# Kernel tuning notes

Hardware: AMD Instinct MI355X
Metric: run time of the kernel (lower is better)

The kernel has to match this reference:

```python
import jax, jax.numpy as jnp
import numpy as np
import itertools
from jax import lax

KERNEL_SIZE = 3
ITERATION = 12
PAD = KERNEL_SIZE // 2
# offsets in the exact order torch code generates them: product([0,1,-1], repeat=2)
OFFSETS = list(itertools.product([*range(KERNEL_SIZE // 2 + 1), *range(-(KERNEL_SIZE // 2), 0)], repeat=2))


def setup_inputs() -> dict:
    key = jax.random.key(0)
    k1, k2, k3, k4 = jax.random.split(key, 4)
    B, C, H, W = 4, 32, 480, 640
    kernel_x = jax.random.normal(k1, (B, C, H, W), jnp.float32)
    x = jax.random.normal(k2, (B, 1, H, W), jnp.float32)
    W_aff = jax.random.normal(k3, (KERNEL_SIZE ** 2 - 1, C, 3, 3), jnp.float32) * 0.05
    b_aff = jax.random.normal(k4, (KERNEL_SIZE ** 2 - 1,), jnp.float32) * 0.05
    return {"kernel_x": kernel_x, "x": x, "W_aff": W_aff, "b_aff": b_aff}


def _gen_kernel(aff):
    # aff: [B, k^2-1, H, W] -> normalized affinity kernel [B, k^2, H, W]
    abs_sum = jnp.sum(jnp.abs(aff), axis=1, keepdims=True)
    a = aff / abs_sum
    s = jnp.sum(a, axis=1, keepdims=True)
    return jnp.concatenate([1.0 - s, a], axis=1)


def _im2col(x):
    # x: [B, 1, H, W] -> shifted copies [B, k^2, H, W] with zero padding,
    # out[:, k, p] = x[:, 0, p - offset_k]
    B, _, H, W = x.shape
    xp = jnp.pad(x[:, 0], ((0, 0), (PAD, PAD), (PAD, PAD)))
    cols = [xp[:, PAD - oi:PAD - oi + H, PAD - oj:PAD - oj + W] for (oi, oj) in OFFSETS]
    return jnp.stack(cols, axis=1)


def reference(kernel_x, x, W_aff, b_aff):
    # affinity_net: 3x3 conv, 32 -> 8 channels, SAME padding
    aff = lax.conv_general_dilated(
        kernel_x, W_aff, window_strides=(1, 1), padding="SAME",
        dimension_numbers=("NCHW", "OIHW", "NCHW"),
    ) + b_aff[None, :, None, None]
    kernel = _gen_kernel(aff)  # [B, 9, H, W]
    for _ in range(ITERATION):
        x = jnp.sum(_im2col(x) * kernel, axis=1, keepdims=True)
    return x
```

## Files before the change

kernel.cpp:

```cpp
#include <hip/hip_runtime.h>
#include <hip/hip_fp16.h>

#define BB 4
#define CC 32
#define HH 480
#define WW 640
#define HWv (HH*WW)

union H8 { __half h[8]; float4 f4; };
union H4 { short4 s; __half h[4]; };

__global__ __launch_bounds__(128) void conv_gen(const float* __restrict__ kx,
                                                const float* __restrict__ Wf,
                                                const float* __restrict__ bf,
                                                __half* __restrict__ K)
{
    int tid = blockIdx.x * 128 + threadIdx.x;
    const int XT = WW / 8;
    int x8 = tid % XT;
    int t2 = tid / XT;
    int y  = t2 % HH;
    int b  = t2 / HH;
    if (b >= BB) return;
    int x0 = x8 * 8;

    float acc[8][8];
#pragma unroll
    for (int o = 0; o < 8; ++o) {
        float bv = bf[o];
#pragma unroll
        for (int p = 0; p < 8; ++p) acc[o][p] = bv;
    }

    const float* kxb = kx + (size_t)b * CC * HWv + (size_t)y * WW + x0;
    const bool xm = (x0 > 0);
    const bool xp = (x0 + 8 < WW);

    for (int c = 0; c < CC; ++c) {
        const float* pl = kxb + (size_t)c * HWv;
#pragma unroll
        for (int r = 0; r < 3; ++r) {
            const int dy = r - 1;
            const bool rowok = (y + dy >= 0) && (y + dy < HH);
            const float* rp = pl + dy * WW;
            float row[10];
            if (rowok) {
                float4 v0 = *reinterpret_cast<const float4*>(rp);
                float4 v1 = *reinterpret_cast<const float4*>(rp + 4);
                row[0] = xm ? rp[-1] : 0.f;
                row[1] = v0.x; row[2] = v0.y; row[3] = v0.z; row[4] = v0.w;
                row[5] = v1.x; row[6] = v1.y; row[7] = v1.z; row[8] = v1.w;
                row[9] = xp ? rp[8] : 0.f;
            } else {
#pragma unroll
                for (int q = 0; q < 10; ++q) row[q] = 0.f;
            }
#pragma unroll
            for (int o = 0; o < 8; ++o) {
#pragma unroll
                for (int t = 0; t < 3; ++t) {
                    float wv = Wf[((o * CC + c) * 3 + r) * 3 + t];
#pragma unroll
                    for (int p = 0; p < 8; ++p) acc[o][p] += wv * row[p + t];
                }
            }
        }
    }

    float k0[8];
#pragma unroll
    for (int p = 0; p < 8; ++p) {
        float asum = 0.f;
#pragma unroll
        for (int o = 0; o < 8; ++o) asum += fabsf(acc[o][p]);
        float rinv = 1.0f / asum;
        float s = 0.f;
#pragma unroll
        for (int o = 0; o < 8; ++o) { acc[o][p] *= rinv; s += acc[o][p]; }
        k0[p] = 1.0f - s;
    }

    size_t base = (size_t)b * 9 * HWv + (size_t)y * WW + x0;
    {
        H8 u;
#pragma unroll
        for (int p = 0; p < 8; ++p) u.h[p] = __float2half(k0[p]);
        *reinterpret_cast<float4*>(K + base) = u.f4;
    }
#pragma unroll
    for (int o = 0; o < 8; ++o) {
        H8 u;
#pragma unroll
        for (int p = 0; p < 8; ++p) u.h[p] = __float2half(acc[o][p]);
        *reinterpret_cast<float4*>(K + base + (size_t)(o + 1) * HWv) = u.f4;
    }
}

__device__ __forceinline__ void load_row6(const float* r, bool rowok, bool xm,
                                          bool xpl, float o[6])
{
    if (rowok) {
        float4 v = *reinterpret_cast<const float4*>(r);
        o[0] = xm ? r[-1] : 0.f;
        o[1] = v.x; o[2] = v.y; o[3] = v.z; o[4] = v.w;
        o[5] = xpl ? r[4] : 0.f;
    } else {
#pragma unroll
        for (int q = 0; q < 6; ++q) o[q] = 0.f;
    }
}

__device__ __forceinline__ void load_row6h(const __half* r, bool rowok, bool xm,
                                           bool xpl, float o[6])
{
    if (rowok) {
        H4 u;
        u.s = *reinterpret_cast<const short4*>(r);
        o[0] = xm ? __half2float(r[-1]) : 0.f;
        o[1] = __half2float(u.h[0]); o[2] = __half2float(u.h[1]);
        o[3] = __half2float(u.h[2]); o[4] = __half2float(u.h[3]);
        o[5] = xpl ? __half2float(r[4]) : 0.f;
    } else {
#pragma unroll
        for (int q = 0; q < 6; ++q) o[q] = 0.f;
    }
}

template <typename TI, typename TO>
__global__ __launch_bounds__(256) void prop(const TI* __restrict__ xin,
                                            const __half* __restrict__ K,
                                            TO* __restrict__ xout)
{
    int tid = blockIdx.x * 256 + threadIdx.x;
    const int XT = WW / 4;
    int x4 = tid % XT;
    int t2 = tid / XT;
    int y  = t2 % HH;
    int b  = t2 / HH;
    if (b >= BB) return;
    int x0 = x4 * 4;

    const bool xm  = (x0 > 0);
    const bool xpl = (x0 + 4 < WW);

    const TI* xb = xin + (size_t)b * HWv + (size_t)y * WW + x0;
    float rm[6], r0[6], rp[6];
    if constexpr (sizeof(TI) == 4) {
        load_row6((const float*)xb - WW, y > 0,      xm, xpl, rm);
        load_row6((const float*)xb,      true,       xm, xpl, r0);
        load_row6((const float*)xb + WW, y < HH - 1, xm, xpl, rp);
    } else {
        load_row6h((const __half*)xb - WW, y > 0,      xm, xpl, rm);
        load_row6h((const __half*)xb,      true,       xm, xpl, r0);
        load_row6h((const __half*)xb + WW, y < HH - 1, xm, xpl, rp);
    }

    const __half* Kb = K + (size_t)b * 9 * HWv + (size_t)y * WW + x0;
    float kv[9][4];
#pragma unroll
    for (int k = 0; k < 9; ++k) {
        H4 u;
        u.s = *reinterpret_cast<const short4*>(Kb + (size_t)k * HWv);
#pragma unroll
        for (int p = 0; p < 4; ++p) kv[k][p] = __half2float(u.h[p]);
    }

    float o4[4];
#pragma unroll
    for (int p = 0; p < 4; ++p) {
        o4[p] = kv[0][p] * r0[p + 1]
              + kv[1][p] * r0[p]
              + kv[2][p] * r0[p + 2]
              + kv[3][p] * rm[p + 1]
              + kv[4][p] * rm[p]
              + kv[5][p] * rm[p + 2]
              + kv[6][p] * rp[p + 1]
              + kv[7][p] * rp[p]
              + kv[8][p] * rp[p + 2];
    }

    TO* ob = xout + (size_t)b * HWv + (size_t)y * WW + x0;
    if constexpr (sizeof(TO) == 4) {
        *reinterpret_cast<float4*>((float*)ob) =
            make_float4(o4[0], o4[1], o4[2], o4[3]);
    } else {
        H4 u;
#pragma unroll
        for (int p = 0; p < 4; ++p) u.h[p] = __float2half(o4[p]);
        *reinterpret_cast<short4*>((__half*)ob) = u.s;
    }
}

extern "C" void kernel_launch(void* const* d_in, const int* in_sizes, int n_in,
                              void* d_out, int out_size, void* d_ws, size_t ws_size,
                              hipStream_t stream) {
    const float* kx   = (const float*)d_in[0];
    const float* x_in = (const float*)d_in[1];
    const float* Wf   = (const float*)d_in[2];
    const float* bf   = (const float*)d_in[3];
    float* out  = (float*)d_out;

    __half* Kbuf = (__half*)d_ws;
    __half* xh0  = Kbuf + (size_t)9 * BB * HWv;
    __half* xh1  = xh0  + (size_t)BB * HWv;
    __half* ping[2] = { xh0, xh1 };

    const int cthreads = BB * HH * (WW / 8);
    conv_gen<<<cthreads / 128, 128, 0, stream>>>(kx, Wf, bf, Kbuf);

    const int pblocks = BB * HH * (WW / 4) / 256;

    prop<float, __half><<<pblocks, 256, 0, stream>>>(x_in, Kbuf, ping[0]);
    for (int it = 1; it <= 10; ++it) {
        prop<__half, __half><<<pblocks, 256, 0, stream>>>(
            ping[(it - 1) & 1], Kbuf, ping[it & 1]);
    }
    prop<__half, float><<<pblocks, 256, 0, stream>>>(ping[0], Kbuf, out);
}
```

Before: 160.0 us.

## Use packed fp16 dot2 instructions for affinity conv with pre-packed weights

Converts the 3x3 conv's input rows and weights to packed half2 pairs across adjacent channels and accumulates them with v_dot2 (fdot2) into fp32. A small pre-kernel packs the weights into half2 form in workspace, and the channel loop now handles two channels per iteration. The goal is to halve the FMA instruction count of the compute-heavy conv. In exchange it adds a conversion step, lowers input precision to fp16, and increases register pressure.

```diff
diff --git a/kernel.cpp b/kernel.cpp
--- a/kernel.cpp
+++ b/kernel.cpp
@@ -7,11 +7,40 @@
 #define WW 640
 #define HWv (HH*WW)
 
+typedef _Float16 half2v __attribute__((ext_vector_type(2)));
+
 union H8 { __half h[8]; float4 f4; };
 union H4 { short4 s; __half h[4]; };
+union PK { float f; half2v h2; };
+
+__device__ __forceinline__ half2v pack2(float a, float b) {
+    PK u;
+    u.f = __builtin_bit_cast(float, __builtin_amdgcn_cvt_pkrtz(a, b));
+    return u.h2;
+}
+
+#if __has_builtin(__builtin_amdgcn_fdot2)
+#define FDOT2(a, b, c) __builtin_amdgcn_fdot2((a), (b), (c), false)
+#else
+#define FDOT2(a, b, c) ((float)(a)[0]*(float)(b)[0] + (float)(a)[1]*(float)(b)[1] + (c))
+#endif
+
+__global__ __launch_bounds__(128) void pack_w(const float* __restrict__ Wf,
+                                              half2v* __restrict__ wpk)
+{
+    for (int i = threadIdx.x; i < (CC / 2) * 8 * 9; i += 128) {
+        int c2  = i / 72;
+        int rem = i - c2 * 72;
+        int o   = rem / 9;
+        int tap = rem - o * 9;
+        float wa = Wf[(o * CC + 2 * c2) * 9 + tap];
+        float wb = Wf[(o * CC + 2 * c2 + 1) * 9 + tap];
+        wpk[i] = pack2(wa, wb);
+    }
+}
 
 __global__ __launch_bounds__(128) void conv_gen(const float* __restrict__ kx,
-                                                const float* __restrict__ Wf,
+                                                const half2v* __restrict__ wpk,
                                                 const float* __restrict__ bf,
                                                 __half* __restrict__ K)
 {
@@ -36,32 +65,55 @@
     const bool xm = (x0 > 0);
     const bool xp = (x0 + 8 < WW);
 
-    for (int c = 0; c < CC; ++c) {
-        const float* pl = kxb + (size_t)c * HWv;
+#pragma unroll 1
+    for (int c2 = 0; c2 < CC / 2; ++c2) {
+        const float* plA = kxb + (size_t)(2 * c2)     * HWv;
+        const float* plB = kxb + (size_t)(2 * c2 + 1) * HWv;
+
+        float rowA[3][10], rowB[3][10];
 #pragma unroll
         for (int r = 0; r < 3; ++r) {
             const int dy = r - 1;
             const bool rowok = (y + dy >= 0) && (y + dy < HH);
-            const float* rp = pl + dy * WW;
-            float row[10];
+            const float* rpA = plA + dy * WW;
+            const float* rpB = plB + dy * WW;
             if (rowok) {
-                float4 v0 = *reinterpret_cast<const float4*>(rp);
-                float4 v1 = *reinterpret_cast<const float4*>(rp + 4);
-                row[0] = xm ? rp[-1] : 0.f;
-                row[1] = v0.x; row[2] = v0.y; row[3] = v0.z; row[4] = v0.w;
-                row[5] = v1.x; row[6] = v1.y; row[7] = v1.z; row[8] = v1.w;
-                row[9] = xp ? rp[8] : 0.f;
+                float4 a0 = *reinterpret_cast<const float4*>(rpA);
+                float4 a1 = *reinterpret_cast<const float4*>(rpA + 4);
+                rowA[r][0] = xm ? rpA[-1] : 0.f;
+                rowA[r][1] = a0.x; rowA[r][2] = a0.y; rowA[r][3] = a0.z; rowA[r][4] = a0.w;
+                rowA[r][5] = a1.x; rowA[r][6] = a1.y; rowA[r][7] = a1.z; rowA[r][8] = a1.w;
+                rowA[r][9] = xp ? rpA[8] : 0.f;
+                float4 b0 = *reinterpret_cast<const float4*>(rpB);
+                float4 b1 = *reinterpret_cast<const float4*>(rpB + 4);
+                rowB[r][0] = xm ? rpB[-1] : 0.f;
+                rowB[r][1] = b0.x; rowB[r][2] = b0.y; rowB[r][3] = b0.z; rowB[r][4] = b0.w;
+                rowB[r][5] = b1.x; rowB[r][6] = b1.y; rowB[r][7] = b1.z; rowB[r][8] = b1.w;
+                rowB[r][9] = xp ? rpB[8] : 0.f;
             } else {
 #pragma unroll
-                for (int q = 0; q < 10; ++q) row[q] = 0.f;
+                for (int q = 0; q < 10; ++q) { rowA[r][q] = 0.f; rowB[r][q] = 0.f; }
             }
-#pragma unroll
-            for (int o = 0; o < 8; ++o) {
+        }
+
+        half2v row2[3][10];
+#pragma unroll
+        for (int r = 0; r < 3; ++r)
+#pragma unroll
+            for (int q = 0; q < 10; ++q)
+                row2[r][q] = pack2(rowA[r][q], rowB[r][q]);
+
+        const half2v* wc = wpk + c2 * 72;
+#pragma unroll
+        for (int o = 0; o < 8; ++o) {
+#pragma unroll
+            for (int r = 0; r < 3; ++r) {
 #pragma unroll
                 for (int t = 0; t < 3; ++t) {
-                    float wv = Wf[((o * CC + c) * 3 + r) * 3 + t];
-#pragma unroll
-                    for (int p = 0; p < 8; ++p) acc[o][p] += wv * row[p + t];
+                    half2v w2 = wc[o * 9 + r * 3 + t];
+#pragma unroll
+                    for (int p = 0; p < 8; ++p)
+                        acc[o][p] = FDOT2(row2[r][p + t], w2, acc[o][p]);
                 }
             }
         }
@@ -200,13 +252,16 @@
     const float* bf   = (const float*)d_in[3];
     float* out  = (float*)d_out;
 
-    __half* Kbuf = (__half*)d_ws;
-    __half* xh0  = Kbuf + (size_t)9 * BB * HWv;
-    __half* xh1  = xh0  + (size_t)BB * HWv;
-    __half* ping[2] = { xh0, xh1 };
+    __half*  Kbuf = (__half*)d_ws;
+    __half*  xh0  = Kbuf + (size_t)9 * BB * HWv;
+    __half*  xh1  = xh0  + (size_t)BB * HWv;
+    half2v*  wpk  = (half2v*)(xh1 + (size_t)BB * HWv);
+    __half*  ping[2] = { xh0, xh1 };
+
+    pack_w<<<1, 128, 0, stream>>>(Wf, wpk);
 
     const int cthreads = BB * HH * (WW / 8);
-    conv_gen<<<cthreads / 128, 128, 0, stream>>>(kx, Wf, bf, Kbuf);
+    conv_gen<<<cthreads / 128, 128, 0, stream>>>(kx, wpk, bf, Kbuf);
 
     const int pblocks = BB * HH * (WW / 4) / 256;
 
```

Measured after the change: 165.3 us. 3.3% more time.

## Replace scalar affinity conv with channel-last fp16 transpose plus MFMA conv

Applied to the files above, without the earlier changes.

The 3x3 32->8 conv drops its per-thread FMA loops. Each batch is first transposed to a channel-last fp16 buffer, and the conv then runs as MFMA 16x16x32 f16 over tiles staged in LDS through global_load_lds. Normalisation uses cross-lane shuffles, and the results are written back through LDS in planar fp16 layout. The aim is to cut the conv's compute cost. In exchange it adds an extra transpose pass per batch, eight serial launches, an fp16 rounding of the inputs and weights, and half of each MFMA tile is wasted on padding columns.

```diff
diff --git a/kernel.cpp b/kernel.cpp
--- a/kernel.cpp
+++ b/kernel.cpp
@@ -7,93 +7,144 @@
 #define WW 640
 #define HWv (HH*WW)
 
-union H8 { __half h[8]; float4 f4; };
+typedef _Float16 f16x8 __attribute__((ext_vector_type(8)));
+typedef float    f32x4 __attribute__((ext_vector_type(4)));
+
 union H4 { short4 s; __half h[4]; };
 
-__global__ __launch_bounds__(128) void conv_gen(const float* __restrict__ kx,
-                                                const float* __restrict__ Wf,
-                                                const float* __restrict__ bf,
-                                                __half* __restrict__ K)
-{
-    int tid = blockIdx.x * 128 + threadIdx.x;
-    const int XT = WW / 8;
-    int x8 = tid % XT;
-    int t2 = tid / XT;
-    int y  = t2 % HH;
-    int b  = t2 / HH;
-    if (b >= BB) return;
-    int x0 = x8 * 8;
-
-    float acc[8][8];
-#pragma unroll
-    for (int o = 0; o < 8; ++o) {
-        float bv = bf[o];
-#pragma unroll
-        for (int p = 0; p < 8; ++p) acc[o][p] = bv;
-    }
-
-    const float* kxb = kx + (size_t)b * CC * HWv + (size_t)y * WW + x0;
-    const bool xm = (x0 > 0);
-    const bool xp = (x0 + 8 < WW);
-
-    for (int c = 0; c < CC; ++c) {
-        const float* pl = kxb + (size_t)c * HWv;
-#pragma unroll
-        for (int r = 0; r < 3; ++r) {
-            const int dy = r - 1;
-            const bool rowok = (y + dy >= 0) && (y + dy < HH);
-            const float* rp = pl + dy * WW;
-            float row[10];
-            if (rowok) {
-                float4 v0 = *reinterpret_cast<const float4*>(rp);
-                float4 v1 = *reinterpret_cast<const float4*>(rp + 4);
-                row[0] = xm ? rp[-1] : 0.f;
-                row[1] = v0.x; row[2] = v0.y; row[3] = v0.z; row[4] = v0.w;
-                row[5] = v1.x; row[6] = v1.y; row[7] = v1.z; row[8] = v1.w;
-                row[9] = xp ? rp[8] : 0.f;
-            } else {
-#pragma unroll
-                for (int q = 0; q < 10; ++q) row[q] = 0.f;
+__global__ __launch_bounds__(256) void tpose(const float* __restrict__ kx_b,
+                                             _Float16* __restrict__ T)
+{
+    int tid = blockIdx.x * 256 + threadIdx.x;
+    const float* src = kx_b + tid;
+    _Float16* dst = T + (size_t)tid * CC;
+
+    f16x8 o[4];
+#pragma unroll
+    for (int g = 0; g < 4; ++g) {
+#pragma unroll
+        for (int j = 0; j < 8; ++j)
+            o[g][j] = (_Float16)src[(size_t)(g * 8 + j) * HWv];
+    }
+#pragma unroll
+    for (int g = 0; g < 4; ++g)
+        *reinterpret_cast<f16x8*>(dst + g * 8) = o[g];
+
+    if (blockIdx.x == 0 && threadIdx.x == 0) {
+        f16x8 z = {};
+        *reinterpret_cast<f16x8*>(T + (size_t)HWv * CC) = z;
+    }
+}
+
+#define CTR 4
+#define CTC 64
+#define SU  1792
+
+__global__ __launch_bounds__(256) void conv_mfma(const _Float16* __restrict__ T,
+                                                 const float* __restrict__ Wf,
+                                                 const float* __restrict__ bf,
+                                                 __half* __restrict__ Kb)
+{
+    __shared__ _Float16 smem[SU * 8];
+
+    const int t    = threadIdx.x;
+    const int lane = t & 63;
+    const int wv   = t >> 6;
+    const int n    = lane & 15;
+    const int ks   = lane >> 4;
+
+    const int xt = blockIdx.x % (WW / CTC);
+    const int yt = blockIdx.x / (WW / CTC);
+    const int y0 = yt * CTR;
+    const int x0 = xt * CTC;
+
+    const _Float16* zpage = T + (size_t)HWv * CC;
+
+    for (int i = wv; i < 28; i += 4) {
+        int u  = i * 64 + lane;
+        int x  = u % 73;
+        int q  = u / 73;
+        int ksu = q & 3;
+        int ry  = q >> 2;
+        int gy = y0 - 1 + ry;
+        int gx = x0 - 4 + x;
+        bool ok = (ry < 6) && (gy >= 0) && (gy < HH) && (gx >= 0) && (gx < WW);
+        const _Float16* src = ok ? (T + ((size_t)gy * WW + gx) * CC + ksu * 8)
+                                 : zpage;
+        __builtin_amdgcn_global_load_lds(
+            (const __attribute__((address_space(1))) void*)src,
+            (__attribute__((address_space(3))) void*)((char*)smem + i * 1024),
+            16, 0, 0);
+    }
+
+    f16x8 btap[9];
+#pragma unroll
+    for (int tp = 0; tp < 9; ++tp) {
+#pragma unroll
+        for (int j = 0; j < 8; ++j) {
+            float w = (n < 8) ? Wf[(n * CC + (ks * 8 + j)) * 9 + tp] : 0.f;
+            btap[tp][j] = (_Float16)w;
+        }
+    }
+    const float bfv = (n < 8) ? bf[n] : 0.f;
+
+    __syncthreads();
+
+    f32x4 acc[4];
+#pragma unroll
+    for (int g = 0; g < 4; ++g) acc[g] = f32x4{bfv, bfv, bfv, bfv};
+
+#pragma unroll
+    for (int g = 0; g < 4; ++g) {
+#pragma unroll
+        for (int ty = 0; ty < 3; ++ty) {
+#pragma unroll
+            for (int tx = 0; tx < 3; ++tx) {
+                int xcol = g * 16 + n + tx + 3;
+                int ryA  = wv + ty;
+                const f16x8* ap = reinterpret_cast<const f16x8*>(
+                    (const char*)smem + ((ryA * 4 + ks) * 73 + xcol) * 16);
+                acc[g] = __builtin_amdgcn_mfma_f32_16x16x32_f16(
+                             *ap, btap[ty * 3 + tx], acc[g], 0, 0, 0);
             }
-#pragma unroll
-            for (int o = 0; o < 8; ++o) {
-#pragma unroll
-                for (int t = 0; t < 3; ++t) {
-                    float wv = Wf[((o * CC + c) * 3 + r) * 3 + t];
-#pragma unroll
-                    for (int p = 0; p < 8; ++p) acc[o][p] += wv * row[p + t];
-                }
+        }
+    }
+    __syncthreads();
+
+    _Float16* outa = smem;
+#pragma unroll
+    for (int g = 0; g < 4; ++g) {
+        float aff[4], sa[4], ss[4];
+#pragma unroll
+        for (int r = 0; r < 4; ++r) {
+            aff[r] = (n < 8) ? acc[g][r] : 0.f;
+            sa[r]  = fabsf(aff[r]);
+            ss[r]  = aff[r];
+        }
+#pragma unroll
+        for (int wdt = 1; wdt <= 4; wdt <<= 1) {
+#pragma unroll
+            for (int r = 0; r < 4; ++r) {
+                sa[r] += __shfl_xor(sa[r], wdt);
+                ss[r] += __shfl_xor(ss[r], wdt);
             }
         }
-    }
-
-    float k0[8];
-#pragma unroll
-    for (int p = 0; p < 8; ++p) {
-        float asum = 0.f;
-#pragma unroll
-        for (int o = 0; o < 8; ++o) asum += fabsf(acc[o][p]);
-        float rinv = 1.0f / asum;
-        float s = 0.f;
-#pragma unroll
-        for (int o = 0; o < 8; ++o) { acc[o][p] *= rinv; s += acc[o][p]; }
-        k0[p] = 1.0f - s;
-    }
-
-    size_t base = (size_t)b * 9 * HWv + (size_t)y * WW + x0;
-    {
-        H8 u;
-#pragma unroll
-        for (int p = 0; p < 8; ++p) u.h[p] = __float2half(k0[p]);
-        *reinterpret_cast<float4*>(K + base) = u.f4;
-    }
-#pragma unroll
-    for (int o = 0; o < 8; ++o) {
-        H8 u;
-#pragma unroll
-        for (int p = 0; p < 8; ++p) u.h[p] = __float2half(acc[o][p]);
-        *reinterpret_cast<float4*>(K + base + (size_t)(o + 1) * HWv) = u.f4;
-    }
+#pragma unroll
+        for (int r = 0; r < 4; ++r) {
+            float rinv = 1.0f / sa[r];
+            float av   = aff[r] * rinv;
+            float k0   = 1.0f - ss[r] * rinv;
+            int px = wv * 64 + g * 16 + ks * 4 + r;
+            if (n < 8)  outa[px * 10 + n + 1] = (_Float16)av;
+            if (n == 0) outa[px * 10 + 0]     = (_Float16)k0;
+        }
+    }
+    __syncthreads();
+
+    __half* Kp = Kb + (size_t)(y0 + (t >> 6)) * WW + x0 + (t & 63);
+#pragma unroll
+    for (int p = 0; p < 9; ++p)
+        Kp[(size_t)p * HWv] = __float2half((float)outa[t * 10 + p]);
 }
 
 __device__ __forceinline__ void load_row6(const float* r, bool rowok, bool xm,
@@ -200,20 +251,26 @@
     const float* bf   = (const float*)d_in[3];
     float* out  = (float*)d_out;
 
-    __half* Kbuf = (__half*)d_ws;
-    __half* xh0  = Kbuf + (size_t)9 * BB * HWv;
-    __half* xh1  = xh0  + (size_t)BB * HWv;
-    __half* ping[2] = { xh0, xh1 };
-
-    const int cthreads = BB * HH * (WW / 8);
-    conv_gen<<<cthreads / 128, 128, 0, stream>>>(kx, Wf, bf, Kbuf);
+    _Float16* Kbuf = (_Float16*)d_ws;
+    _Float16* xh0  = Kbuf + (size_t)9 * BB * HWv;
+    _Float16* xh1  = xh0  + (size_t)BB * HWv;
+    _Float16* T    = xh1  + (size_t)BB * HWv;
+    __half* KbufH  = (__half*)Kbuf;
+    __half* ping[2] = { (__half*)xh0, (__half*)xh1 };
+
+    const int tblocks = HWv / 256;
+    const int cblocks = (HH / CTR) * (WW / CTC);
+    for (int b = 0; b < BB; ++b) {
+        tpose<<<tblocks, 256, 0, stream>>>(kx + (size_t)b * CC * HWv, T);
+        conv_mfma<<<cblocks, 256, 0, stream>>>(T, Wf, bf,
+                                               KbufH + (size_t)b * 9 * HWv);
+    }
 
     const int pblocks = BB * HH * (WW / 4) / 256;
-
-    prop<float, __half><<<pblocks, 256, 0, stream>>>(x_in, Kbuf, ping[0]);
+    prop<float, __half><<<pblocks, 256, 0, stream>>>(x_in, KbufH, ping[0]);
     for (int it = 1; it <= 10; ++it) {
         prop<__half, __half><<<pblocks, 256, 0, stream>>>(
-            ping[(it - 1) & 1], Kbuf, ping[it & 1]);
-    }
-    prop<__half, float><<<pblocks, 256, 0, stream>>>(ping[0], Kbuf, out);
-}
+            ping[(it - 1) & 1], KbufH, ping[it & 1]);
+    }
+    prop<__half, float><<<pblocks, 256, 0, stream>>>(ping[0], KbufH, out);
+}
```

New measurement: 268.1 us. +67.6%, slower.

## Retile conv_gen to 4-pixel threads in 2D blocks with shuffle halos

Applied to the files above, without the earlier changes.

Each conv_gen thread now computes 4 pixels instead of 8, and each 128-thread block covers a 4-row by 128-column tile. Left and right halo values are obtained with wavefront shuffles rather than separate scalar loads, and boundary handling uses multiplicative masks instead of branches. The channel loop is kept rolled. The intent is to cut register pressure from the 8x8 accumulator, raising occupancy, and to reduce redundant edge loads. The cost is more threads and more repeated weight loads per pixel. The shuffles assume a 32-lane grouping, but on a 64-wide wavefront lanes 31 and 32 are still neighbours, so the tx==0 and tx==31 fallbacks stay correct.

```diff
diff --git a/kernel.cpp b/kernel.cpp
--- a/kernel.cpp
+++ b/kernel.cpp
@@ -15,61 +15,79 @@
                                                 const float* __restrict__ bf,
                                                 __half* __restrict__ K)
 {
-    int tid = blockIdx.x * 128 + threadIdx.x;
-    const int XT = WW / 8;
-    int x8 = tid % XT;
-    int t2 = tid / XT;
-    int y  = t2 % HH;
-    int b  = t2 / HH;
-    if (b >= BB) return;
-    int x0 = x8 * 8;
-
-    float acc[8][8];
+    const int t  = threadIdx.x;
+    const int tx = t & 31;
+    const int ty = t >> 5;
+    int blk = blockIdx.x;
+    const int xt = blk % (WW / 128); blk /= (WW / 128);
+    const int yt = blk % (HH / 4);
+    const int b  = blk / (HH / 4);
+    const int y  = yt * 4 + ty;
+    const int x0 = xt * 128 + 4 * tx;
+
+    float acc[8][4];
 #pragma unroll
     for (int o = 0; o < 8; ++o) {
         float bv = bf[o];
 #pragma unroll
-        for (int p = 0; p < 8; ++p) acc[o][p] = bv;
+        for (int p = 0; p < 4; ++p) acc[o][p] = bv;
     }
 
     const float* kxb = kx + (size_t)b * CC * HWv + (size_t)y * WW + x0;
+
     const bool xm = (x0 > 0);
-    const bool xp = (x0 + 8 < WW);
-
+    const bool xp = (x0 + 4 < WW);
+    const float xmf = xm ? 1.f : 0.f;
+    const float xpf = xp ? 1.f : 0.f;
+    const int eoffl = xm ? -1 : 0;
+    const int eoffr = xp ?  4 : 3;
+
+    int   rowoff[3];
+    float mc[3];
+#pragma unroll
+    for (int r = 0; r < 3; ++r) {
+        int dy = r - 1;
+        bool ok = (y + dy >= 0) && (y + dy < HH);
+        rowoff[r] = ok ? dy * WW : 0;
+        mc[r] = ok ? 1.f : 0.f;
+    }
+
+#pragma unroll 1
     for (int c = 0; c < CC; ++c) {
         const float* pl = kxb + (size_t)c * HWv;
+
+        float row[3][6];
 #pragma unroll
         for (int r = 0; r < 3; ++r) {
-            const int dy = r - 1;
-            const bool rowok = (y + dy >= 0) && (y + dy < HH);
-            const float* rp = pl + dy * WW;
-            float row[10];
-            if (rowok) {
-                float4 v0 = *reinterpret_cast<const float4*>(rp);
-                float4 v1 = *reinterpret_cast<const float4*>(rp + 4);
-                row[0] = xm ? rp[-1] : 0.f;
-                row[1] = v0.x; row[2] = v0.y; row[3] = v0.z; row[4] = v0.w;
-                row[5] = v1.x; row[6] = v1.y; row[7] = v1.z; row[8] = v1.w;
-                row[9] = xp ? rp[8] : 0.f;
-            } else {
-#pragma unroll
-                for (int q = 0; q < 10; ++q) row[q] = 0.f;
-            }
-#pragma unroll
-            for (int o = 0; o < 8; ++o) {
-#pragma unroll
-                for (int t = 0; t < 3; ++t) {
-                    float wv = Wf[((o * CC + c) * 3 + r) * 3 + t];
-#pragma unroll
-                    for (int p = 0; p < 8; ++p) acc[o][p] += wv * row[p + t];
+            const float* rp = pl + rowoff[r];
+            float4 v = *reinterpret_cast<const float4*>(rp);
+            float lv = __shfl_up(v.w, 1);
+            float rv = __shfl_down(v.x, 1);
+            if (tx == 0)  lv = rp[eoffl] * xmf;
+            if (tx == 31) rv = rp[eoffr] * xpf;
+            row[r][0] = lv  * mc[r];
+            row[r][1] = v.x * mc[r]; row[r][2] = v.y * mc[r];
+            row[r][3] = v.z * mc[r]; row[r][4] = v.w * mc[r];
+            row[r][5] = rv  * mc[r];
+        }
+
+#pragma unroll
+        for (int o = 0; o < 8; ++o) {
+#pragma unroll
+            for (int r = 0; r < 3; ++r) {
+#pragma unroll
+                for (int s = 0; s < 3; ++s) {
+                    float wv = Wf[((o * CC + c) * 3 + r) * 3 + s];
+#pragma unroll
+                    for (int p = 0; p < 4; ++p) acc[o][p] += wv * row[r][p + s];
                 }
             }
         }
     }
 
-    float k0[8];
-#pragma unroll
-    for (int p = 0; p < 8; ++p) {
+    float k0[4];
+#pragma unroll
+    for (int p = 0; p < 4; ++p) {
         float asum = 0.f;
 #pragma unroll
         for (int o = 0; o < 8; ++o) asum += fabsf(acc[o][p]);
@@ -82,17 +100,17 @@
 
     size_t base = (size_t)b * 9 * HWv + (size_t)y * WW + x0;
     {
-        H8 u;
-#pragma unroll
-        for (int p = 0; p < 8; ++p) u.h[p] = __float2half(k0[p]);
-        *reinterpret_cast<float4*>(K + base) = u.f4;
+        H4 u;
+#pragma unroll
+        for (int p = 0; p < 4; ++p) u.h[p] = __float2half(k0[p]);
+        *reinterpret_cast<short4*>(K + base) = u.s;
     }
 #pragma unroll
     for (int o = 0; o < 8; ++o) {
-        H8 u;
-#pragma unroll
-        for (int p = 0; p < 8; ++p) u.h[p] = __float2half(acc[o][p]);
-        *reinterpret_cast<float4*>(K + base + (size_t)(o + 1) * HWv) = u.f4;
+        H4 u;
+#pragma unroll
+        for (int p = 0; p < 4; ++p) u.h[p] = __float2half(acc[o][p]);
+        *reinterpret_cast<short4*>(K + base + (size_t)(o + 1) * HWv) = u.s;
     }
 }
 
@@ -205,8 +223,8 @@
     __half* xh1  = xh0  + (size_t)BB * HWv;
     __half* ping[2] = { xh0, xh1 };
 
-    const int cthreads = BB * HH * (WW / 8);
-    conv_gen<<<cthreads / 128, 128, 0, stream>>>(kx, Wf, bf, Kbuf);
+    const int cblocks = BB * (HH / 4) * (WW / 128);
+    conv_gen<<<cblocks, 128, 0, stream>>>(kx, Wf, bf, Kbuf);
 
     const int pblocks = BB * HH * (WW / 4) / 256;
 
```

Result: slower. 270.5 us (+69.1%).
